# Performance work log

Measured on AMD Instinct MI355X. Metric: run time of the kernel, lower is better.

Reference implementation:

```python
import jax, jax.numpy as jnp
import numpy as np

DIMS = 2048
Q_HEADS = 32
K_HEADS = 8
HEAD_DIM = DIMS // Q_HEADS  # 64
KV_DIM = K_HEADS * HEAD_DIM  # 512
B, S, IN_DIM = 2, 2048, 2048


def setup_inputs() -> dict:
    key = jax.random.key(0)
    ks = jax.random.split(key, 11)
    sc_in = 1.0 / np.sqrt(IN_DIM)
    sc_out = 1.0 / np.sqrt(DIMS)
    return {
        "q": jax.random.normal(ks[0], (B, S, IN_DIM), jnp.float32),
        "k": jax.random.normal(ks[1], (B, S, IN_DIM), jnp.float32),
        "v": jax.random.normal(ks[2], (B, S, IN_DIM), jnp.float32),
        "Wq": jax.random.normal(ks[3], (IN_DIM, DIMS), jnp.float32) * sc_in,
        "bq": jnp.zeros((DIMS,), jnp.float32),
        "Wk": jax.random.normal(ks[4], (IN_DIM, KV_DIM), jnp.float32) * sc_in,
        "bk": jnp.zeros((KV_DIM,), jnp.float32),
        "Wv": jax.random.normal(ks[5], (IN_DIM, KV_DIM), jnp.float32) * sc_in,
        "bv": jnp.zeros((KV_DIM,), jnp.float32),
        "Wo": jax.random.normal(ks[6], (DIMS, IN_DIM), jnp.float32) * sc_out,
        "bo": jnp.zeros((IN_DIM,), jnp.float32),
    }


def reference(q, k, v, Wq, bq, Wk, bk, Wv, bv, Wo, bo):
    rep = Q_HEADS // K_HEADS
    # projections
    qx = (q @ Wq + bq).reshape(B, S, Q_HEADS, HEAD_DIM)
    kx = (k @ Wk + bk).reshape(B, S, K_HEADS, HEAD_DIM)
    vx = (v @ Wv + bv).reshape(B, S, K_HEADS, HEAD_DIM)
    # repeat kv heads to match q heads (matches kx.repeat(rep, axis=-2))
    kx = jnp.repeat(kx, rep, axis=-2)
    vx = jnpp_repeat(vx, rep) if False else jnp.repeat(vx, rep, axis=-2)
    # [B, H, S, D]
    qx = jnp.einsum('bshd->bhsd', qx)
    kx = jnp.einsum('bshd->bhsd', kx)
    vx = jnp.einsum('bshd->bhsd', vx)
    scores = jnp.einsum('bhqd,bhkd->bhqk', qx, kx) / jnp.sqrt(
        jnp.asarray(HEAD_DIM, qx.dtype))
    scores = jax.nn.softmax(scores, axis=-1)
    out = jnp.einsum('bhqk,bhkd->bhqd', scores, vx)
    out = jnp.einsum('bhsd->bshd', out).reshape(B, S, DIMS)
    return out @ Wo + bo
```

## Files before the change

kernel.cpp:

```cpp
#include <hip/hip_runtime.h>
#include <cstdint>
#include <cstddef>

typedef _Float16 half8   __attribute__((ext_vector_type(8)));
typedef _Float16 half4_t __attribute__((ext_vector_type(4)));
typedef __fp16   fp16x2  __attribute__((ext_vector_type(2)));
typedef float    f32x4   __attribute__((ext_vector_type(4)));

typedef __attribute__((address_space(1))) const void GV;
typedef __attribute__((address_space(3))) void LV;

__device__ __forceinline__ void gl_lds16(const _Float16* g, _Float16* l) {
    __builtin_amdgcn_global_load_lds((GV*)g, (LV*)l, 16, 0, 0);
}

#define BB    2
#define SS    2048
#define INDIM 2048
#define DIMS_ 2048
#define QH    32
#define KH_   8
#define HD    64
#define KVD   512
#define RWS   4096

#define QSCALE (0.125f * 1.44269504088896340736f)

__global__ void cast_f16_3(const float* __restrict__ a, const float* __restrict__ b,
                           const float* __restrict__ c,
                           _Float16* __restrict__ oa, _Float16* __restrict__ ob,
                           _Float16* __restrict__ oc) {
    const float* in  = (blockIdx.y == 0) ? a : (blockIdx.y == 1) ? b : c;
    _Float16*    out = (blockIdx.y == 0) ? oa : (blockIdx.y == 1) ? ob : oc;
    int i = (blockIdx.x * 256 + threadIdx.x) * 8;
    const float4* p = (const float4*)(in + i);
    float4 x = p[0], y = p[1];
    half8 h;
    h[0]=(_Float16)x.x; h[1]=(_Float16)x.y; h[2]=(_Float16)x.z; h[3]=(_Float16)x.w;
    h[4]=(_Float16)y.x; h[5]=(_Float16)y.y; h[6]=(_Float16)y.z; h[7]=(_Float16)y.w;
    *(half8*)(out + i) = h;
}

__global__ void transpose_cast2(const float* __restrict__ in0, _Float16* __restrict__ out0,
                                const float* __restrict__ in1, _Float16* __restrict__ out1,
                                int R, int C) {
    const float* in  = blockIdx.z ? in1 : in0;
    _Float16*    out = blockIdx.z ? out1 : out0;
    __shared__ float t[32][33];
    int r0 = blockIdx.y * 32, c0 = blockIdx.x * 32;
    int tx = threadIdx.x, ty = threadIdx.y;
    for (int i = ty; i < 32; i += 8)
        t[i][tx] = in[(size_t)(r0 + i) * C + c0 + tx];
    __syncthreads();
    for (int i = ty; i < 32; i += 8)
        out[(size_t)(c0 + i) * R + r0 + tx] = (_Float16)t[tx][i];
}

__global__ __launch_bounds__(256) void gemm_qkv(
    const _Float16* __restrict__ q16, const _Float16* __restrict__ k16,
    const _Float16* __restrict__ v16,
    const _Float16* __restrict__ WqT, const _Float16* __restrict__ WkT,
    const _Float16* __restrict__ WvT,
    const float* __restrict__ bq, const float* __restrict__ bk,
    const float* __restrict__ bv,
    _Float16* __restrict__ qx, _Float16* __restrict__ kx,
    _Float16* __restrict__ vtg)
{
    const int bid = blockIdx.x;
    const _Float16* A; const _Float16* Bt; const float* bias;
    int bn, bm, N, mode; float scale;
    if (bid < 512)      { mode = 0; A = q16; Bt = WqT; bias = bq; N = 2048;
                          bn = bid & 15; bm = bid >> 4; scale = QSCALE; }
    else if (bid < 640) { int t = bid - 512; mode = 1; A = k16; Bt = WkT; bias = bk;
                          N = 512; bn = t & 3; bm = t >> 2; scale = 1.0f; }
    else                { int t = bid - 640; mode = 2; A = v16; Bt = WvT; bias = bv;
                          N = 512; bn = t & 3; bm = t >> 2; scale = 1.0f; }
    const int K = 2048;

    const int tid = threadIdx.x;
    const int wave = tid >> 6, lane = tid & 63, quad = lane >> 4, l15 = lane & 15;
    const int wm = wave & 1, wn = wave >> 1;

    __shared__ __align__(16) _Float16 As[128 * 32];
    __shared__ __align__(16) _Float16 Bs[128 * 32];

    f32x4 acc[4][4] = {};

    for (int kt = 0; kt < K / 32; ++kt) {
        __syncthreads();
        const _Float16* Ag = A  + (size_t)(bm * 128) * K + kt * 32;
        const _Float16* Bg = Bt + (size_t)(bn * 128) * K + kt * 32;
#pragma unroll
        for (int i = 0; i < 2; ++i) {
            int f = i * 256 + tid;
            gl_lds16(Ag + (size_t)(f >> 2) * K + (f & 3) * 8,
                     As + (size_t)(i * 256 + (tid & 192)) * 8);
            gl_lds16(Bg + (size_t)(f >> 2) * K + (f & 3) * 8,
                     Bs + (size_t)(i * 256 + (tid & 192)) * 8);
        }
        __syncthreads();

        half8 af[4], bf[4];
#pragma unroll
        for (int i = 0; i < 4; ++i)
            af[i] = *(const half8*)(As + (wm * 64 + i * 16 + l15) * 32 + quad * 8);
#pragma unroll
        for (int j = 0; j < 4; ++j)
            bf[j] = *(const half8*)(Bs + (wn * 64 + j * 16 + l15) * 32 + quad * 8);
#pragma unroll
        for (int i = 0; i < 4; ++i)
#pragma unroll
            for (int j = 0; j < 4; ++j)
                acc[i][j] = __builtin_amdgcn_mfma_f32_16x16x32_f16(af[i], bf[j], acc[i][j], 0, 0, 0);
    }

    const int row0 = bm * 128 + wm * 64;
    const int col0 = bn * 128 + wn * 64;
    if (mode < 2) {
        _Float16* out = mode ? kx : qx;
#pragma unroll
        for (int j = 0; j < 4; ++j) {
            int col = col0 + j * 16 + l15;
            float bv_ = bias[col];
#pragma unroll
            for (int i = 0; i < 4; ++i)
#pragma unroll
                for (int r = 0; r < 4; ++r) {
                    int row = row0 + i * 16 + quad * 4 + r;
                    out[(size_t)row * N + col] = (_Float16)((acc[i][j][r] + bv_) * scale);
                }
        }
    } else {
#pragma unroll
        for (int j = 0; j < 4; ++j) {
            int c = col0 + j * 16 + l15;
            int kh = c >> 6, d = c & 63;
            float bv_ = bias[c];
#pragma unroll
            for (int i = 0; i < 4; ++i) {
                int row = row0 + i * 16 + quad * 4;
                int bb2 = row >> 11, s = row & 2047;
                half4_t hp;
#pragma unroll
                for (int r = 0; r < 4; ++r) hp[r] = (_Float16)(acc[i][j][r] + bv_);
                *(half4_t*)(vtg + ((size_t)(bb2 * KH_ + kh) * HD + d) * SS + s) = hp;
            }
        }
    }
}

__global__ __launch_bounds__(256) void gemm_oproj(
    const _Float16* __restrict__ A, const _Float16* __restrict__ Bt,
    const float* __restrict__ bias, float* __restrict__ Cf)
{
    const int N = 2048, K = 2048;
    const int bn = blockIdx.x, bm = blockIdx.y;
    const int tid = threadIdx.x;
    const int wave = tid >> 6, lane = tid & 63, quad = lane >> 4, l15 = lane & 15;
    const int wm = wave & 1, wn = wave >> 1;

    __shared__ __align__(16) _Float16 As[128 * 32];
    __shared__ __align__(16) _Float16 Bs[128 * 32];

    f32x4 acc[4][4] = {};

    for (int kt = 0; kt < K / 32; ++kt) {
        __syncthreads();
        const _Float16* Ag = A  + (size_t)(bm * 128) * K + kt * 32;
        const _Float16* Bg = Bt + (size_t)(bn * 128) * K + kt * 32;
#pragma unroll
        for (int i = 0; i < 2; ++i) {
            int f = i * 256 + tid;
            gl_lds16(Ag + (size_t)(f >> 2) * K + (f & 3) * 8,
                     As + (size_t)(i * 256 + (tid & 192)) * 8);
            gl_lds16(Bg + (size_t)(f >> 2) * K + (f & 3) * 8,
                     Bs + (size_t)(i * 256 + (tid & 192)) * 8);
        }
        __syncthreads();

        half8 af[4], bf[4];
#pragma unroll
        for (int i = 0; i < 4; ++i)
            af[i] = *(const half8*)(As + (wm * 64 + i * 16 + l15) * 32 + quad * 8);
#pragma unroll
        for (int j = 0; j < 4; ++j)
            bf[j] = *(const half8*)(Bs + (wn * 64 + j * 16 + l15) * 32 + quad * 8);
#pragma unroll
        for (int i = 0; i < 4; ++i)
#pragma unroll
            for (int j = 0; j < 4; ++j)
                acc[i][j] = __builtin_amdgcn_mfma_f32_16x16x32_f16(af[i], bf[j], acc[i][j], 0, 0, 0);
    }

    const int row0 = bm * 128 + wm * 64;
    const int col0 = bn * 128 + wn * 64;
#pragma unroll
    for (int j = 0; j < 4; ++j) {
        int col = col0 + j * 16 + l15;
        float bv_ = bias[col];
#pragma unroll
        for (int i = 0; i < 4; ++i)
#pragma unroll
            for (int r = 0; r < 4; ++r) {
                int row = row0 + i * 16 + quad * 4 + r;
                Cf[(size_t)row * N + col] = acc[i][j][r] + bv_;
            }
    }
}

__global__ __launch_bounds__(256, 2) void attn_fused(
    const _Float16* __restrict__ qx, const _Float16* __restrict__ kx,
    const _Float16* __restrict__ vt, _Float16* __restrict__ o16)
{
    const int qt = blockIdx.x;
    const int bh = blockIdx.y;
    const int bb = bh >> 5, h = bh & 31, kh = h >> 2;
    const int tid = threadIdx.x;
    const int w = tid >> 6, lane = tid & 63, quad = lane >> 4, l15 = lane & 15;

    __shared__ __align__(16) _Float16 Ks[64 * 64];
    __shared__ __align__(16) _Float16 Vs[64 * 64];
    __shared__ __align__(16) _Float16 Ps[4][64 * 72];

    const size_t qrow0 = (size_t)bb * SS + (size_t)qt * 256 + w * 64;
    half8 qf[4][2];
#pragma unroll
    for (int nb = 0; nb < 4; ++nb)
#pragma unroll
        for (int kk = 0; kk < 2; ++kk)
            qf[nb][kk] = *(const half8*)(qx + (qrow0 + nb * 16 + l15) * DIMS_
                                            + h * HD + kk * 32 + quad * 8);

    half8 vone;
#pragma unroll
    for (int i = 0; i < 8; ++i) vone[i] = (_Float16)1.0f;

    f32x4 ob[4][4] = {};
    f32x4 lacc[4] = {};

    const _Float16* kbase = kx + (size_t)bb * SS * KVD + kh * HD;
    const _Float16* vbase = vt + (size_t)(bb * KH_ + kh) * HD * SS;
    _Float16* Pw = &Ps[w][0];

    const int srowlo = lane >> 3;
    const int scol   = ((lane & 7) ^ srowlo) * 8;

    for (int kt = 0; kt < SS / 64; ++kt) {
        __syncthreads();
#pragma unroll
        for (int i = 0; i < 2; ++i) {
            int row = w * 16 + i * 8 + srowlo;
            gl_lds16(kbase + (size_t)(kt * 64 + row) * KVD + scol,
                     Ks + (w * 16 + i * 8) * 64);
            gl_lds16(vbase + (size_t)row * SS + kt * 64 + scol,
                     Vs + (w * 16 + i * 8) * 64);
        }
        __syncthreads();

#pragma unroll
        for (int mk = 0; mk < 4; ++mk) {
            f32x4 st4[4] = {};
#pragma unroll
            for (int kk = 0; kk < 2; ++kk) {
                half8 ka = *(const half8*)(Ks + (mk * 16 + l15) * 64
                                              + (((kk * 4 + quad) ^ (l15 & 7)) * 8));
#pragma unroll
                for (int nb = 0; nb < 4; ++nb)
                    st4[nb] = __builtin_amdgcn_mfma_f32_16x16x32_f16(
                        ka, qf[nb][kk], st4[nb], 0, 0, 0);
            }
#pragma unroll
            for (int nb = 0; nb < 4; ++nb) {
                float p0 = __builtin_amdgcn_exp2f(st4[nb][0]);
                float p1 = __builtin_amdgcn_exp2f(st4[nb][1]);
                float p2 = __builtin_amdgcn_exp2f(st4[nb][2]);
                float p3 = __builtin_amdgcn_exp2f(st4[nb][3]);
                fp16x2 lo = __builtin_amdgcn_cvt_pkrtz(p0, p1);
                fp16x2 hi = __builtin_amdgcn_cvt_pkrtz(p2, p3);
                half4_t hp;
                hp[0] = (_Float16)lo[0]; hp[1] = (_Float16)lo[1];
                hp[2] = (_Float16)hi[0]; hp[3] = (_Float16)hi[1];
                *(half4_t*)(Pw + (nb * 16 + l15) * 72 + mk * 16 + quad * 4) = hp;
            }
        }

#pragma unroll
        for (int kk = 0; kk < 2; ++kk) {
            half8 pa[4], vb[4];
#pragma unroll
            for (int mb = 0; mb < 4; ++mb)
                pa[mb] = *(const half8*)(Pw + (mb * 16 + l15) * 72 + kk * 32 + quad * 8);
#pragma unroll
            for (int nd = 0; nd < 4; ++nd)
                vb[nd] = *(const half8*)(Vs + (nd * 16 + l15) * 64
                                            + (((kk * 4 + quad) ^ (l15 & 7)) * 8));
#pragma unroll
            for (int mb = 0; mb < 4; ++mb) {
#pragma unroll
                for (int nd = 0; nd < 4; ++nd)
                    ob[mb][nd] = __builtin_amdgcn_mfma_f32_16x16x32_f16(
                        pa[mb], vb[nd], ob[mb][nd], 0, 0, 0);
                lacc[mb] = __builtin_amdgcn_mfma_f32_16x16x32_f16(
                    pa[mb], vone, lacc[mb], 0, 0, 0);
            }
        }
    }

#pragma unroll
    for (int mb = 0; mb < 4; ++mb)
#pragma unroll
        for (int r = 0; r < 4; ++r) {
            float rl = __builtin_amdgcn_rcpf(lacc[mb][r]);
            size_t row = qrow0 + mb * 16 + quad * 4 + r;
#pragma unroll
            for (int nd = 0; nd < 4; ++nd)
                o16[row * DIMS_ + h * HD + nd * 16 + l15] =
                    (_Float16)(ob[mb][nd][r] * rl);
        }
}

extern "C" void kernel_launch(void* const* d_in, const int* in_sizes, int n_in,
                              void* d_out, int out_size, void* d_ws, size_t ws_size,
                              hipStream_t stream) {
    const float* q  = (const float*)d_in[0];
    const float* k  = (const float*)d_in[1];
    const float* v  = (const float*)d_in[2];
    const float* Wq = (const float*)d_in[3];
    const float* bq = (const float*)d_in[4];
    const float* Wk = (const float*)d_in[5];
    const float* bk = (const float*)d_in[6];
    const float* Wv = (const float*)d_in[7];
    const float* bv = (const float*)d_in[8];
    const float* Wo = (const float*)d_in[9];
    const float* bo = (const float*)d_in[10];

    char* ws = (char*)d_ws;
    _Float16* q16  = (_Float16*)ws;  ws += (size_t)RWS * INDIM * 2;
    _Float16* k16  = (_Float16*)ws;  ws += (size_t)RWS * INDIM * 2;
    _Float16* v16  = (_Float16*)ws;  ws += (size_t)RWS * INDIM * 2;
    _Float16* qx16 = (_Float16*)ws;  ws += (size_t)RWS * DIMS_ * 2;
    _Float16* kx16 = (_Float16*)ws;  ws += (size_t)RWS * KVD * 2;
    _Float16* o16  = (_Float16*)ws;  ws += (size_t)RWS * DIMS_ * 2;
    _Float16* WqT  = (_Float16*)ws;  ws += (size_t)DIMS_ * INDIM * 2;
    _Float16* WkT  = (_Float16*)ws;  ws += (size_t)KVD * INDIM * 2;
    _Float16* WvT  = (_Float16*)ws;  ws += (size_t)KVD * INDIM * 2;
    _Float16* WoT  = (_Float16*)ws;  ws += (size_t)INDIM * DIMS_ * 2;
    _Float16* vtg  = (_Float16*)ws;  ws += (size_t)BB * KH_ * HD * SS * 2;

    const int nAct = RWS * INDIM;
    cast_f16_3<<<dim3(nAct / (256 * 8), 3), 256, 0, stream>>>(q, k, v, q16, k16, v16);

    transpose_cast2<<<dim3(DIMS_ / 32, INDIM / 32, 2), dim3(32, 8), 0, stream>>>(
        Wq, WqT, Wo, WoT, INDIM, DIMS_);
    transpose_cast2<<<dim3(KVD / 32, INDIM / 32, 2), dim3(32, 8), 0, stream>>>(
        Wk, WkT, Wv, WvT, INDIM, KVD);

    gemm_qkv<<<768, 256, 0, stream>>>(q16, k16, v16, WqT, WkT, WvT,
                                      bq, bk, bv, qx16, kx16, vtg);

    attn_fused<<<dim3(SS / 256, BB * QH), 256, 0, stream>>>(qx16, kx16, vtg, o16);

    gemm_oproj<<<dim3(INDIM / 128, RWS / 128), 256, 0, stream>>>(
        o16, WoT, bo, (float*)d_out);
}
```

Baseline: 389.0 us.

## Double-buffer LDS tiles in GEMMs and attention with single-barrier prefetch

All three kernels (the QKV projection GEMM, the output-projection GEMM and fused attention) now keep two LDS buffers for their global-to-LDS tiles. Each iteration issues the async load for tile kt+1 right after one barrier and then computes on tile kt, so global load latency overlaps with MFMA work and one of the two barriers per iteration goes away. The attention P scratch buffer also drops its padded 72-element row stride for a 64-element stride with an XOR swizzle, so the larger double-buffered K/V tiles still fit in LDS without bank conflicts. The cost is twice the tile LDS footprint, which could limit occupancy. Correctness also depends on the barrier waiting for the outstanding async LDS loads.

Result: slower. 402.1 us (+3.4%).

```diff
diff --git a/kernel.cpp b/kernel.cpp
--- a/kernel.cpp
+++ b/kernel.cpp
@@ -81,32 +81,43 @@
     const int wave = tid >> 6, lane = tid & 63, quad = lane >> 4, l15 = lane & 15;
     const int wm = wave & 1, wn = wave >> 1;
 
-    __shared__ __align__(16) _Float16 As[128 * 32];
-    __shared__ __align__(16) _Float16 Bs[128 * 32];
+    __shared__ __align__(16) _Float16 As[2][128 * 32];
+    __shared__ __align__(16) _Float16 Bs[2][128 * 32];
 
     f32x4 acc[4][4] = {};
 
-    for (int kt = 0; kt < K / 32; ++kt) {
+    const int f0 = tid, f1 = 256 + tid;
+    const size_t arow0 = (size_t)(f0 >> 2) * K + (f0 & 3) * 8;
+    const size_t arow1 = (size_t)(f1 >> 2) * K + (f1 & 3) * 8;
+    const int ldst0 = (tid & 192) * 8, ldst1 = (256 + (tid & 192)) * 8;
+    const _Float16* Ab = A  + (size_t)(bm * 128) * K;
+    const _Float16* Bb = Bt + (size_t)(bn * 128) * K;
+
+#define QKV_STAGE(kt, buf)                                             \
+    {                                                                  \
+        const _Float16* Ag = Ab + (kt) * 32;                           \
+        const _Float16* Bg = Bb + (kt) * 32;                           \
+        gl_lds16(Ag + arow0, As[buf] + ldst0);                         \
+        gl_lds16(Ag + arow1, As[buf] + ldst1);                         \
+        gl_lds16(Bg + arow0, Bs[buf] + ldst0);                         \
+        gl_lds16(Bg + arow1, Bs[buf] + ldst1);                         \
+    }
+
+    QKV_STAGE(0, 0);
+    const int kiters = K >> 5;
+    for (int kt = 0; kt < kiters; ++kt) {
         __syncthreads();
-        const _Float16* Ag = A  + (size_t)(bm * 128) * K + kt * 32;
-        const _Float16* Bg = Bt + (size_t)(bn * 128) * K + kt * 32;
-#pragma unroll
-        for (int i = 0; i < 2; ++i) {
-            int f = i * 256 + tid;
-            gl_lds16(Ag + (size_t)(f >> 2) * K + (f & 3) * 8,
-                     As + (size_t)(i * 256 + (tid & 192)) * 8);
-            gl_lds16(Bg + (size_t)(f >> 2) * K + (f & 3) * 8,
-                     Bs + (size_t)(i * 256 + (tid & 192)) * 8);
-        }
-        __syncthreads();
+        if (kt + 1 < kiters) QKV_STAGE(kt + 1, (kt + 1) & 1);
+        const _Float16* Asb = As[kt & 1];
+        const _Float16* Bsb = Bs[kt & 1];
 
         half8 af[4], bf[4];
 #pragma unroll
         for (int i = 0; i < 4; ++i)
-            af[i] = *(const half8*)(As + (wm * 64 + i * 16 + l15) * 32 + quad * 8);
+            af[i] = *(const half8*)(Asb + (wm * 64 + i * 16 + l15) * 32 + quad * 8);
 #pragma unroll
         for (int j = 0; j < 4; ++j)
-            bf[j] = *(const half8*)(Bs + (wn * 64 + j * 16 + l15) * 32 + quad * 8);
+            bf[j] = *(const half8*)(Bsb + (wn * 64 + j * 16 + l15) * 32 + quad * 8);
 #pragma unroll
         for (int i = 0; i < 4; ++i)
 #pragma unroll
@@ -159,32 +170,33 @@
     const int wave = tid >> 6, lane = tid & 63, quad = lane >> 4, l15 = lane & 15;
     const int wm = wave & 1, wn = wave >> 1;
 
-    __shared__ __align__(16) _Float16 As[128 * 32];
-    __shared__ __align__(16) _Float16 Bs[128 * 32];
+    __shared__ __align__(16) _Float16 As[2][128 * 32];
+    __shared__ __align__(16) _Float16 Bs[2][128 * 32];
 
     f32x4 acc[4][4] = {};
 
-    for (int kt = 0; kt < K / 32; ++kt) {
+    const int f0 = tid, f1 = 256 + tid;
+    const size_t arow0 = (size_t)(f0 >> 2) * K + (f0 & 3) * 8;
+    const size_t arow1 = (size_t)(f1 >> 2) * K + (f1 & 3) * 8;
+    const int ldst0 = (tid & 192) * 8, ldst1 = (256 + (tid & 192)) * 8;
+    const _Float16* Ab = A  + (size_t)(bm * 128) * K;
+    const _Float16* Bb = Bt + (size_t)(bn * 128) * K;
+
+    QKV_STAGE(0, 0);
+    const int kiters = K >> 5;
+    for (int kt = 0; kt < kiters; ++kt) {
         __syncthreads();
-        const _Float16* Ag = A  + (size_t)(bm * 128) * K + kt * 32;
-        const _Float16* Bg = Bt + (size_t)(bn * 128) * K + kt * 32;
-#pragma unroll
-        for (int i = 0; i < 2; ++i) {
-            int f = i * 256 + tid;
-            gl_lds16(Ag + (size_t)(f >> 2) * K + (f & 3) * 8,
-                     As + (size_t)(i * 256 + (tid & 192)) * 8);
-            gl_lds16(Bg + (size_t)(f >> 2) * K + (f & 3) * 8,
-                     Bs + (size_t)(i * 256 + (tid & 192)) * 8);
-        }
-        __syncthreads();
+        if (kt + 1 < kiters) QKV_STAGE(kt + 1, (kt + 1) & 1);
+        const _Float16* Asb = As[kt & 1];
+        const _Float16* Bsb = Bs[kt & 1];
 
         half8 af[4], bf[4];
 #pragma unroll
         for (int i = 0; i < 4; ++i)
-            af[i] = *(const half8*)(As + (wm * 64 + i * 16 + l15) * 32 + quad * 8);
+            af[i] = *(const half8*)(Asb + (wm * 64 + i * 16 + l15) * 32 + quad * 8);
 #pragma unroll
         for (int j = 0; j < 4; ++j)
-            bf[j] = *(const half8*)(Bs + (wn * 64 + j * 16 + l15) * 32 + quad * 8);
+            bf[j] = *(const half8*)(Bsb + (wn * 64 + j * 16 + l15) * 32 + quad * 8);
 #pragma unroll
         for (int i = 0; i < 4; ++i)
 #pragma unroll
@@ -218,9 +230,31 @@
     const int tid = threadIdx.x;
     const int w = tid >> 6, lane = tid & 63, quad = lane >> 4, l15 = lane & 15;
 
-    __shared__ __align__(16) _Float16 Ks[64 * 64];
-    __shared__ __align__(16) _Float16 Vs[64 * 64];
-    __shared__ __align__(16) _Float16 Ps[4][64 * 72];
+    __shared__ __align__(16) _Float16 Ks[2][64 * 64];
+    __shared__ __align__(16) _Float16 Vs[2][64 * 64];
+    __shared__ __align__(16) _Float16 Ps[4][64 * 64];
+
+    const _Float16* kbase = kx + (size_t)bb * SS * KVD + kh * HD;
+    const _Float16* vbase = vt + (size_t)(bb * KH_ + kh) * HD * SS;
+    _Float16* Pw = &Ps[w][0];
+
+    const int srowlo = lane >> 3;
+    const int scol   = ((lane & 7) ^ srowlo) * 8;
+
+#define ATTN_STAGE(kt, buf)                                                  \
+    {                                                                        \
+        _Float16* Kd = &Ks[buf][0]; _Float16* Vd = &Vs[buf][0];              \
+        _Pragma("unroll")                                                    \
+        for (int i = 0; i < 2; ++i) {                                        \
+            int row = w * 16 + i * 8 + srowlo;                               \
+            gl_lds16(kbase + (size_t)((kt) * 64 + row) * KVD + scol,         \
+                     Kd + (w * 16 + i * 8) * 64);                            \
+            gl_lds16(vbase + (size_t)row * SS + (kt) * 64 + scol,            \
+                     Vd + (w * 16 + i * 8) * 64);                            \
+        }                                                                    \
+    }
+
+    ATTN_STAGE(0, 0);
 
     const size_t qrow0 = (size_t)bb * SS + (size_t)qt * 256 + w * 64;
     half8 qf[4][2];
@@ -238,37 +272,26 @@
     f32x4 ob[4][4] = {};
     f32x4 lacc[4] = {};
 
-    const _Float16* kbase = kx + (size_t)bb * SS * KVD + kh * HD;
-    const _Float16* vbase = vt + (size_t)(bb * KH_ + kh) * HD * SS;
-    _Float16* Pw = &Ps[w][0];
-
-    const int srowlo = lane >> 3;
-    const int scol   = ((lane & 7) ^ srowlo) * 8;
-
     for (int kt = 0; kt < SS / 64; ++kt) {
         __syncthreads();
-#pragma unroll
-        for (int i = 0; i < 2; ++i) {
-            int row = w * 16 + i * 8 + srowlo;
-            gl_lds16(kbase + (size_t)(kt * 64 + row) * KVD + scol,
-                     Ks + (w * 16 + i * 8) * 64);
-            gl_lds16(vbase + (size_t)row * SS + kt * 64 + scol,
-                     Vs + (w * 16 + i * 8) * 64);
-        }
-        __syncthreads();
+        if (kt + 1 < SS / 64) ATTN_STAGE(kt + 1, (kt + 1) & 1);
+        const _Float16* Ksb = &Ks[kt & 1][0];
+        const _Float16* Vsb = &Vs[kt & 1][0];
 
 #pragma unroll
         for (int mk = 0; mk < 4; ++mk) {
             f32x4 st4[4] = {};
 #pragma unroll
             for (int kk = 0; kk < 2; ++kk) {
-                half8 ka = *(const half8*)(Ks + (mk * 16 + l15) * 64
+                half8 ka = *(const half8*)(Ksb + (mk * 16 + l15) * 64
                                               + (((kk * 4 + quad) ^ (l15 & 7)) * 8));
 #pragma unroll
                 for (int nb = 0; nb < 4; ++nb)
                     st4[nb] = __builtin_amdgcn_mfma_f32_16x16x32_f16(
                         ka, qf[nb][kk], st4[nb], 0, 0, 0);
             }
+            const int pcolbase = (quad & 1) * 4;
+            const int pgrp = mk * 2 + (quad >> 1);
 #pragma unroll
             for (int nb = 0; nb < 4; ++nb) {
                 float p0 = __builtin_amdgcn_exp2f(st4[nb][0]);
@@ -280,7 +303,8 @@
                 half4_t hp;
                 hp[0] = (_Float16)lo[0]; hp[1] = (_Float16)lo[1];
                 hp[2] = (_Float16)hi[0]; hp[3] = (_Float16)hi[1];
-                *(half4_t*)(Pw + (nb * 16 + l15) * 72 + mk * 16 + quad * 4) = hp;
+                *(half4_t*)(Pw + (nb * 16 + l15) * 64
+                               + ((pgrp ^ (l15 & 7)) * 8) + pcolbase) = hp;
             }
         }
 
@@ -289,10 +313,11 @@
             half8 pa[4], vb[4];
 #pragma unroll
             for (int mb = 0; mb < 4; ++mb)
-                pa[mb] = *(const half8*)(Pw + (mb * 16 + l15) * 72 + kk * 32 + quad * 8);
+                pa[mb] = *(const half8*)(Pw + (mb * 16 + l15) * 64
+                                            + (((kk * 4 + quad) ^ (l15 & 7)) * 8));
 #pragma unroll
             for (int nd = 0; nd < 4; ++nd)
-                vb[nd] = *(const half8*)(Vs + (nd * 16 + l15) * 64
+                vb[nd] = *(const half8*)(Vsb + (nd * 16 + l15) * 64
                                             + (((kk * 4 + quad) ^ (l15 & 7)) * 8));
 #pragma unroll
             for (int mb = 0; mb < 4; ++mb) {
```
